# Optimization experiments

Measured on AMD Instinct MI355X. Metric: run time of the kernel, lower is better.

## Reference

```python
import jax, jax.numpy as jnp
import numpy as np

NUM_FREQ = 32  # feat_dim // 4
DSZ = 4


def _freq_matrices(L_params, D_params, U_params):
    """Reconstruct per-frequency 4x4 matrices M = L @ diag(exp(D)) @ U from LDU params."""
    n = L_params.shape[0]
    eye = jnp.eye(DSZ, dtype=L_params.dtype)
    L = jnp.tile(eye[None], (n, 1, 1))
    L = (L.at[:, 1, 0].set(L_params[:, 0])
          .at[:, 2, 0].set(L_params[:, 1])
          .at[:, 2, 1].set(L_params[:, 2])
          .at[:, 3, 0].set(L_params[:, 3])
          .at[:, 3, 1].set(L_params[:, 4])
          .at[:, 3, 2].set(L_params[:, 5]))
    U = jnp.tile(eye[None], (n, 1, 1))
    U = (U.at[:, 0, 1].set(U_params[:, 0])
          .at[:, 0, 2].set(U_params[:, 1])
          .at[:, 0, 3].set(U_params[:, 2])
          .at[:, 1, 2].set(U_params[:, 3])
          .at[:, 1, 3].set(U_params[:, 4])
          .at[:, 2, 3].set(U_params[:, 5]))
    # L @ diag(exp(D)) @ U, batched over frequency
    return jnp.einsum('fij,fj,fjk->fik', L, jnp.exp(D_params), U)


def setup_inputs() -> dict:
    key = jax.random.key(0)
    k1, k2, k3, k4, k5 = jax.random.split(key, 5)
    feats = jax.random.normal(k1, (4, 16, 4096, 128), dtype=jnp.float32)
    matrix = jax.random.normal(k2, (4, 8, 4, 4), dtype=jnp.float32)
    L_params = 0.1 * jax.random.normal(k3, (NUM_FREQ, 6), dtype=jnp.float32)
    # rand_scale init: D = log(rand*1.5 + 0.5)
    D_params = jnp.log(jax.random.uniform(k4, (NUM_FREQ, 4), dtype=jnp.float32) * 1.5 + 0.5)
    U_params = 0.1 * jax.random.normal(k5, (NUM_FREQ, 6), dtype=jnp.float32)
    return {"feats": feats, "matrix": matrix, "L_params": L_params,
            "D_params": D_params, "U_params": U_params}


def reference(feats, matrix, L_params, D_params, U_params):
    # apply_tiled_projmat with pos_enc='prope', type='LDU', side='left',
    # transpose=False, inverse=False.
    freq = _freq_matrices(L_params, D_params, U_params)          # [F,4,4]
    m5 = jnp.einsum('fij,bcjk->bcfik', freq, matrix)             # [B,C,F,4,4]
    b, n, s, fd = feats.shape
    c = matrix.shape[1]
    p = s // c
    f = feats.reshape(b, n, c, p, NUM_FREQ, DSZ)
    out = jnp.einsum('bcfij,bncpfj->bncpfi', m5, f)
    return out.reshape(b, n, s, fd)
```

## Files before the change

kernel.cpp:

```cpp
#include <hip/hip_runtime.h>

#define NUM_FREQ 32
#define B_DIM 4
#define N_DIM 16
#define S_DIM 4096
#define FD_DIM 128
#define C_DIM 8
#define P_DIM 512

__global__ void build_m5_kernel(const float* __restrict__ matrix,
                                const float* __restrict__ L_params,
                                const float* __restrict__ D_params,
                                const float* __restrict__ U_params,
                                float* __restrict__ m5) {
    int idx = blockIdx.x * blockDim.x + threadIdx.x;
    const int total = B_DIM * C_DIM * NUM_FREQ;
    if (idx >= total) return;

    int f  = idx & (NUM_FREQ - 1);
    int bc = idx >> 5;

    const float l0 = L_params[f * 6 + 0];
    const float l1 = L_params[f * 6 + 1];
    const float l2 = L_params[f * 6 + 2];
    const float l3 = L_params[f * 6 + 3];
    const float l4 = L_params[f * 6 + 4];
    const float l5 = L_params[f * 6 + 5];

    const float e0 = __expf(D_params[f * 4 + 0]);
    const float e1 = __expf(D_params[f * 4 + 1]);
    const float e2 = __expf(D_params[f * 4 + 2]);
    const float e3 = __expf(D_params[f * 4 + 3]);

    const float u0 = U_params[f * 6 + 0];
    const float u1 = U_params[f * 6 + 1];
    const float u2 = U_params[f * 6 + 2];
    const float u3 = U_params[f * 6 + 3];
    const float u4 = U_params[f * 6 + 4];
    const float u5 = U_params[f * 6 + 5];

    float fr[4][4];
    fr[0][0] = e0;       fr[0][1] = e0 * u0;  fr[0][2] = e0 * u1;          fr[0][3] = e0 * u2;
    fr[1][0] = l0 * e0;
    fr[1][1] = l0 * e0 * u0 + e1;
    fr[1][2] = l0 * e0 * u1 + e1 * u3;
    fr[1][3] = l0 * e0 * u2 + e1 * u4;
    fr[2][0] = l1 * e0;
    fr[2][1] = l1 * e0 * u0 + l2 * e1;
    fr[2][2] = l1 * e0 * u1 + l2 * e1 * u3 + e2;
    fr[2][3] = l1 * e0 * u2 + l2 * e1 * u4 + e2 * u5;
    fr[3][0] = l3 * e0;
    fr[3][1] = l3 * e0 * u0 + l4 * e1;
    fr[3][2] = l3 * e0 * u1 + l4 * e1 * u3 + l5 * e2;
    fr[3][3] = l3 * e0 * u2 + l4 * e1 * u4 + l5 * e2 * u5 + e3;

    const float* mt = matrix + bc * 16;
    float* out = m5 + idx * 16;
#pragma unroll
    for (int i = 0; i < 4; ++i) {
#pragma unroll
        for (int k = 0; k < 4; ++k) {
            out[i * 4 + k] = fr[i][0] * mt[0 * 4 + k]
                           + fr[i][1] * mt[1 * 4 + k]
                           + fr[i][2] * mt[2 * 4 + k]
                           + fr[i][3] * mt[3 * 4 + k];
        }
    }
}

__global__ void __launch_bounds__(256)
apply_kernel(const float4* __restrict__ feats,
             const float* __restrict__ m5,
             float4* __restrict__ out) {
    const int idx = blockIdx.x * blockDim.x + threadIdx.x;

    const int f  = idx & 31;
    const int sp = idx >> 5;
    const int s  = sp & 4095;
    const int b  = sp >> 16;
    const int c  = s >> 9;

    const float4* M = reinterpret_cast<const float4*>(
        m5 + ((((b << 3) + c) << 5) + f) * 16);
    const float4 m0 = M[0];
    const float4 m1 = M[1];
    const float4 m2 = M[2];
    const float4 m3 = M[3];

    const float4 v = feats[idx];
    float4 o;
    o.x = m0.x * v.x + m0.y * v.y + m0.z * v.z + m0.w * v.w;
    o.y = m1.x * v.x + m1.y * v.y + m1.z * v.z + m1.w * v.w;
    o.z = m2.x * v.x + m2.y * v.y + m2.z * v.z + m2.w * v.w;
    o.w = m3.x * v.x + m3.y * v.y + m3.z * v.z + m3.w * v.w;
    out[idx] = o;
}

extern "C" void kernel_launch(void* const* d_in, const int* in_sizes, int n_in,
                              void* d_out, int out_size, void* d_ws, size_t ws_size,
                              hipStream_t stream) {
    const float* feats    = (const float*)d_in[0];
    const float* matrix   = (const float*)d_in[1];
    const float* L_params = (const float*)d_in[2];
    const float* D_params = (const float*)d_in[3];
    const float* U_params = (const float*)d_in[4];
    float* out = (float*)d_out;
    float* m5  = (float*)d_ws;

    build_m5_kernel<<<4, 256, 0, stream>>>(matrix, L_params, D_params, U_params, m5);

    const int total4 = (B_DIM * N_DIM * S_DIM * FD_DIM) / 4;
    const int block = 256;
    const int grid = total4 / block;
    apply_kernel<<<grid, block, 0, stream>>>(
        reinterpret_cast<const float4*>(feats), m5,
        reinterpret_cast<float4*>(out));
}
```

Baseline: 49.52 us.

## Fuse matrix build into apply kernel with shared-memory matrices and nontemporal I/O

Drops the separate build kernel. Each block now recomputes its 32 per-frequency 4x4 matrices into shared memory, and each thread then handles four float4 elements instead of one. Loads are issued before the matrix build so the memory latency overlaps it, and loads and stores use nontemporal hints to avoid polluting the cache. This removes a kernel launch, the workspace round trip, and the repeated global matrix loads. The cost is redundant per-block parameter math and a __syncthreads barrier. Correctness relies on every block's 1024 float4 elements sharing the same b and c.

```diff
diff --git a/kernel.cpp b/kernel.cpp
--- a/kernel.cpp
+++ b/kernel.cpp
@@ -1,99 +1,90 @@
 #include <hip/hip_runtime.h>
 
 #define NUM_FREQ 32
-#define B_DIM 4
-#define N_DIM 16
-#define S_DIM 4096
-#define FD_DIM 128
-#define C_DIM 8
-#define P_DIM 512
+#define KU 4
 
-__global__ void build_m5_kernel(const float* __restrict__ matrix,
-                                const float* __restrict__ L_params,
-                                const float* __restrict__ D_params,
-                                const float* __restrict__ U_params,
-                                float* __restrict__ m5) {
-    int idx = blockIdx.x * blockDim.x + threadIdx.x;
-    const int total = B_DIM * C_DIM * NUM_FREQ;
-    if (idx >= total) return;
+typedef float vfloat4 __attribute__((ext_vector_type(4)));
 
-    int f  = idx & (NUM_FREQ - 1);
-    int bc = idx >> 5;
+__global__ void __launch_bounds__(256)
+camfreq_fused_kernel(const vfloat4* __restrict__ feats,
+                     const float* __restrict__ matrix,
+                     const float* __restrict__ L_params,
+                     const float* __restrict__ D_params,
+                     const float* __restrict__ U_params,
+                     vfloat4* __restrict__ out) {
+    __shared__ float m5[16][NUM_FREQ];
 
-    const float l0 = L_params[f * 6 + 0];
-    const float l1 = L_params[f * 6 + 1];
-    const float l2 = L_params[f * 6 + 2];
-    const float l3 = L_params[f * 6 + 3];
-    const float l4 = L_params[f * 6 + 4];
-    const float l5 = L_params[f * 6 + 5];
+    const int t = threadIdx.x;
+    const int base = blockIdx.x * (256 * KU);
 
-    const float e0 = __expf(D_params[f * 4 + 0]);
-    const float e1 = __expf(D_params[f * 4 + 1]);
-    const float e2 = __expf(D_params[f * 4 + 2]);
-    const float e3 = __expf(D_params[f * 4 + 3]);
+    const int sp0 = base >> 5;
+    const int s0  = sp0 & 4095;
+    const int b   = sp0 >> 16;
+    const int c   = s0 >> 9;
 
-    const float u0 = U_params[f * 6 + 0];
-    const float u1 = U_params[f * 6 + 1];
-    const float u2 = U_params[f * 6 + 2];
-    const float u3 = U_params[f * 6 + 3];
-    const float u4 = U_params[f * 6 + 4];
-    const float u5 = U_params[f * 6 + 5];
+    vfloat4 v[KU];
+#pragma unroll
+    for (int k = 0; k < KU; ++k) {
+        v[k] = __builtin_nontemporal_load(&feats[base + k * 256 + t]);
+    }
 
-    float fr[4][4];
-    fr[0][0] = e0;       fr[0][1] = e0 * u0;  fr[0][2] = e0 * u1;          fr[0][3] = e0 * u2;
-    fr[1][0] = l0 * e0;
-    fr[1][1] = l0 * e0 * u0 + e1;
-    fr[1][2] = l0 * e0 * u1 + e1 * u3;
-    fr[1][3] = l0 * e0 * u2 + e1 * u4;
-    fr[2][0] = l1 * e0;
-    fr[2][1] = l1 * e0 * u0 + l2 * e1;
-    fr[2][2] = l1 * e0 * u1 + l2 * e1 * u3 + e2;
-    fr[2][3] = l1 * e0 * u2 + l2 * e1 * u4 + e2 * u5;
-    fr[3][0] = l3 * e0;
-    fr[3][1] = l3 * e0 * u0 + l4 * e1;
-    fr[3][2] = l3 * e0 * u1 + l4 * e1 * u3 + l5 * e2;
-    fr[3][3] = l3 * e0 * u2 + l4 * e1 * u4 + l5 * e2 * u5 + e3;
+    if (t < NUM_FREQ) {
+        const int f = t;
+        const float l0 = L_params[f * 6 + 0], l1 = L_params[f * 6 + 1];
+        const float l2 = L_params[f * 6 + 2], l3 = L_params[f * 6 + 3];
+        const float l4 = L_params[f * 6 + 4], l5 = L_params[f * 6 + 5];
+        const float e0 = __expf(D_params[f * 4 + 0]);
+        const float e1 = __expf(D_params[f * 4 + 1]);
+        const float e2 = __expf(D_params[f * 4 + 2]);
+        const float e3 = __expf(D_params[f * 4 + 3]);
+        const float u0 = U_params[f * 6 + 0], u1 = U_params[f * 6 + 1];
+        const float u2 = U_params[f * 6 + 2], u3 = U_params[f * 6 + 3];
+        const float u4 = U_params[f * 6 + 4], u5 = U_params[f * 6 + 5];
 
-    const float* mt = matrix + bc * 16;
-    float* out = m5 + idx * 16;
+        float fr[4][4];
+        fr[0][0] = e0;      fr[0][1] = e0 * u0;       fr[0][2] = e0 * u1;                 fr[0][3] = e0 * u2;
+        fr[1][0] = l0 * e0;
+        fr[1][1] = l0 * e0 * u0 + e1;
+        fr[1][2] = l0 * e0 * u1 + e1 * u3;
+        fr[1][3] = l0 * e0 * u2 + e1 * u4;
+        fr[2][0] = l1 * e0;
+        fr[2][1] = l1 * e0 * u0 + l2 * e1;
+        fr[2][2] = l1 * e0 * u1 + l2 * e1 * u3 + e2;
+        fr[2][3] = l1 * e0 * u2 + l2 * e1 * u4 + e2 * u5;
+        fr[3][0] = l3 * e0;
+        fr[3][1] = l3 * e0 * u0 + l4 * e1;
+        fr[3][2] = l3 * e0 * u1 + l4 * e1 * u3 + l5 * e2;
+        fr[3][3] = l3 * e0 * u2 + l4 * e1 * u4 + l5 * e2 * u5 + e3;
+
+        const float* mt = matrix + ((b << 3) + c) * 16;
 #pragma unroll
-    for (int i = 0; i < 4; ++i) {
+        for (int i = 0; i < 4; ++i) {
 #pragma unroll
-        for (int k = 0; k < 4; ++k) {
-            out[i * 4 + k] = fr[i][0] * mt[0 * 4 + k]
-                           + fr[i][1] * mt[1 * 4 + k]
-                           + fr[i][2] * mt[2 * 4 + k]
-                           + fr[i][3] * mt[3 * 4 + k];
+            for (int k = 0; k < 4; ++k) {
+                m5[i * 4 + k][f] = fr[i][0] * mt[0 * 4 + k]
+                                 + fr[i][1] * mt[1 * 4 + k]
+                                 + fr[i][2] * mt[2 * 4 + k]
+                                 + fr[i][3] * mt[3 * 4 + k];
+            }
         }
     }
-}
+    __syncthreads();
 
-__global__ void __launch_bounds__(256)
-apply_kernel(const float4* __restrict__ feats,
-             const float* __restrict__ m5,
-             float4* __restrict__ out) {
-    const int idx = blockIdx.x * blockDim.x + threadIdx.x;
+    const int f = t & (NUM_FREQ - 1);
+    const float m00 = m5[ 0][f], m01 = m5[ 1][f], m02 = m5[ 2][f], m03 = m5[ 3][f];
+    const float m10 = m5[ 4][f], m11 = m5[ 5][f], m12 = m5[ 6][f], m13 = m5[ 7][f];
+    const float m20 = m5[ 8][f], m21 = m5[ 9][f], m22 = m5[10][f], m23 = m5[11][f];
+    const float m30 = m5[12][f], m31 = m5[13][f], m32 = m5[14][f], m33 = m5[15][f];
 
-    const int f  = idx & 31;
-    const int sp = idx >> 5;
-    const int s  = sp & 4095;
-    const int b  = sp >> 16;
-    const int c  = s >> 9;
-
-    const float4* M = reinterpret_cast<const float4*>(
-        m5 + ((((b << 3) + c) << 5) + f) * 16);
-    const float4 m0 = M[0];
-    const float4 m1 = M[1];
-    const float4 m2 = M[2];
-    const float4 m3 = M[3];
-
-    const float4 v = feats[idx];
-    float4 o;
-    o.x = m0.x * v.x + m0.y * v.y + m0.z * v.z + m0.w * v.w;
-    o.y = m1.x * v.x + m1.y * v.y + m1.z * v.z + m1.w * v.w;
-    o.z = m2.x * v.x + m2.y * v.y + m2.z * v.z + m2.w * v.w;
-    o.w = m3.x * v.x + m3.y * v.y + m3.z * v.z + m3.w * v.w;
-    out[idx] = o;
+#pragma unroll
+    for (int k = 0; k < KU; ++k) {
+        vfloat4 o;
+        o.x = m00 * v[k].x + m01 * v[k].y + m02 * v[k].z + m03 * v[k].w;
+        o.y = m10 * v[k].x + m11 * v[k].y + m12 * v[k].z + m13 * v[k].w;
+        o.z = m20 * v[k].x + m21 * v[k].y + m22 * v[k].z + m23 * v[k].w;
+        o.w = m30 * v[k].x + m31 * v[k].y + m32 * v[k].z + m33 * v[k].w;
+        __builtin_nontemporal_store(o, &out[base + k * 256 + t]);
+    }
 }
 
 extern "C" void kernel_launch(void* const* d_in, const int* in_sizes, int n_in,
@@ -105,14 +96,11 @@
     const float* D_params = (const float*)d_in[3];
     const float* U_params = (const float*)d_in[4];
     float* out = (float*)d_out;
-    float* m5  = (float*)d_ws;
 
-    build_m5_kernel<<<4, 256, 0, stream>>>(matrix, L_params, D_params, U_params, m5);
-
-    const int total4 = (B_DIM * N_DIM * S_DIM * FD_DIM) / 4;
-    const int block = 256;
-    const int grid = total4 / block;
-    apply_kernel<<<grid, block, 0, stream>>>(
-        reinterpret_cast<const float4*>(feats), m5,
-        reinterpret_cast<float4*>(out));
+    const int total4 = (4 * 16 * 4096 * 128) / 4;
+    const int block  = 256;
+    const int grid   = total4 / (block * KU);
+    camfreq_fused_kernel<<<grid, block, 0, stream>>>(
+        reinterpret_cast<const vfloat4*>(feats), matrix, L_params, D_params,
+        U_params, reinterpret_cast<vfloat4*>(out));
 }
```

After: 46.83 us. 5.4% less time.
